# Performance work log

Hardware: AMD Instinct MI355X
Metric: run time of the kernel (lower is better)

## Reference

```python
import jax, jax.numpy as jnp
import numpy as np

N = 50000
E = 800000
IN_FEATS = 128
OUT_FEATS = 16
EDGE_FEATS = 1
NUM_HEADS = 8


def setup_inputs() -> dict:
    key = jax.random.key(0)
    ks = jax.random.split(key, 8)

    def xavier(k, shape):
        fan_in, fan_out = shape[-1], shape[-2] if len(shape) > 1 else shape[-1]
        bound = float(np.sqrt(6.0 / (shape[0] + shape[1])))
        return jax.random.uniform(k, shape, jnp.float32, -bound, bound)

    h = jax.random.normal(ks[0], (N, IN_FEATS), jnp.float32)
    edge_index = jax.random.randint(ks[1], (2, E), 0, N, jnp.int32)
    edge_feat = jax.random.normal(ks[2], (E, EDGE_FEATS), jnp.float32)
    # W_node stored as [in_feats, out_feats*num_heads] so h @ W_node == torch Linear(h)
    W_node = xavier(ks[3], (IN_FEATS, OUT_FEATS * NUM_HEADS))
    W_edge = xavier(ks[4], (EDGE_FEATS, NUM_HEADS))
    a_src = xavier(ks[5], (NUM_HEADS, OUT_FEATS))
    a_dst = xavier(ks[6], (NUM_HEADS, OUT_FEATS))
    return {"h": h, "edge_index": edge_index, "edge_feat": edge_feat,
            "W_node": W_node, "W_edge": W_edge, "a_src": a_src, "a_dst": a_dst}


def reference(h, edge_index, edge_feat, W_node, W_edge, a_src, a_dst):
    n = h.shape[0]
    src, dst = edge_index[0], edge_index[1]
    # node projection: [N, H, F]
    h_trans = (h @ W_node).reshape(n, NUM_HEADS, OUT_FEATS)
    # edge projection: [E, H]
    e_trans = edge_feat @ W_edge
    src_feat = h_trans[src]  # [E, H, F]
    dst_feat = h_trans[dst]  # [E, H, F]
    attn = (src_feat * a_src).sum(-1) + (dst_feat * a_dst).sum(-1) + e_trans  # [E, H]
    attn = jax.nn.leaky_relu(attn, negative_slope=0.2)
    # segment softmax over edges grouped by dst
    max_val = jax.ops.segment_max(attn, dst, num_segments=n)  # [N, H]
    exp_attn = jnp.exp(attn - max_val[dst])
    sum_exp = jax.ops.segment_sum(exp_attn, dst, num_segments=n)  # [N, H]
    alpha = exp_attn / jnp.maximum(sum_exp[dst], 1e-12)  # [E, H]
    msg = src_feat * alpha[..., None]  # [E, H, F]
    out = jax.ops.segment_sum(msg, dst, num_segments=n)  # [N, H, F]
    return out.mean(axis=1)  # [N, F]
```

## Files before the change

### kernel.cpp

```cpp
#include <hip/hip_runtime.h>

#define N_NODES 50000
#define N_EDGES 800000
#define IN_F    128
#define HEADS   8
#define OUT_F   16
#define NB_PROJ 782
#define NB_HIST 3125

typedef unsigned short u16;
typedef __attribute__((ext_vector_type(8))) short bf16x8;
typedef __attribute__((ext_vector_type(4))) float f32x4;

__device__ __forceinline__ float bf2f(u16 u) {
    return __uint_as_float(((unsigned)u) << 16);
}
__device__ __forceinline__ u16 f2bf(float f) {
    unsigned u = __float_as_uint(f);
    unsigned r = 0x7fffu + ((u >> 16) & 1u);
    return (u16)((u + r) >> 16);
}
__device__ __forceinline__ float ldf(const void* p, int i, bool bf) {
    return bf ? bf2f(((const u16*)p)[i]) : ((const float*)p)[i];
}

__global__ void probe_dtype(const void* __restrict__ h, int* __restrict__ flag) {
    if (threadIdx.x == 0 && blockIdx.x == 0) {
        const u16* u = (const u16*)h;
        int cnt = 0;
        for (int i = 0; i < 128; ++i) {
            int e = (u[i] >> 7) & 0xFF;
            if (e >= 90 && e <= 141) cnt++;
        }
        *flag = (cnt >= 110) ? 1 : 0;
    }
}

#define WT_STRIDE 136
__global__ __launch_bounds__(256) void proj_hist(
    const void* __restrict__ h, const void* __restrict__ Wn,
    const void* __restrict__ a_srcp, const void* __restrict__ a_dstp,
    const int* __restrict__ flag, const int* __restrict__ ei,
    u16* __restrict__ ht, float* __restrict__ s_src, float* __restrict__ s_dst,
    int* __restrict__ deg, int* __restrict__ rank)
{
    if (blockIdx.x >= NB_PROJ) {
        int e = (blockIdx.x - NB_PROJ) * 256 + threadIdx.x;
        if (e < N_EDGES) rank[e] = atomicAdd(&deg[ei[N_EDGES + e]], 1);
        return;
    }

    const bool bf = (*flag) != 0;
    __shared__ u16 Wsh[IN_F * WT_STRIDE];
    __shared__ float a_sh[2][IN_F];
    const int tid = threadIdx.x;

    if (tid < 128) a_sh[0][tid] = ldf(a_srcp, tid, bf);
    else           a_sh[1][tid - 128] = ldf(a_dstp, tid - 128, bf);

    {
        const int c8  = (tid & 15) * 8;
        const int kof = tid >> 4;
        const int ksw = (tid & 7) << 3;
        bf16x8 wv[8];
        if (bf) {
            const u16* wp = (const u16*)Wn;
            #pragma unroll
            for (int j = 0; j < 8; ++j)
                wv[j] = *(const bf16x8*)(wp + (size_t)(j * 16 + kof) * IN_F + c8);
        } else {
            const float* wp = (const float*)Wn;
            #pragma unroll
            for (int j = 0; j < 8; ++j) {
                const float* rp = wp + (size_t)(j * 16 + kof) * IN_F + c8;
                float4 fa = *(const float4*)(rp);
                float4 fb = *(const float4*)(rp + 4);
                bf16x8 t;
                t[0] = (short)f2bf(fa.x); t[1] = (short)f2bf(fa.y);
                t[2] = (short)f2bf(fa.z); t[3] = (short)f2bf(fa.w);
                t[4] = (short)f2bf(fb.x); t[5] = (short)f2bf(fb.y);
                t[6] = (short)f2bf(fb.z); t[7] = (short)f2bf(fb.w);
                wv[j] = t;
            }
        }
        #pragma unroll
        for (int j = 0; j < 8; ++j) {
            int kk = (j * 16 + kof) ^ ksw;
            #pragma unroll
            for (int jj = 0; jj < 8; ++jj)
                Wsh[(c8 + jj) * WT_STRIDE + kk] = (u16)wv[j][jj];
        }
    }
    __syncthreads();

    const int wave = tid >> 6, lane = tid & 63;
    const int m = lane & 15, q = lane >> 4;
    const int row_t = blockIdx.x * 64 + wave * 16;

    bf16x8 afr[4];
    int arow = row_t + m;
    if (arow >= N_NODES) arow = N_NODES - 1;
    if (bf) {
        const u16* hp = (const u16*)h + (size_t)arow * IN_F;
        #pragma unroll
        for (int kt = 0; kt < 4; ++kt)
            afr[kt] = *(const bf16x8*)(hp + kt * 32 + q * 8);
    } else {
        const float* hp = (const float*)h + (size_t)arow * IN_F;
        #pragma unroll
        for (int kt = 0; kt < 4; ++kt) {
            bf16x8 t;
            #pragma unroll
            for (int j = 0; j < 8; ++j) t[j] = (short)f2bf(hp[kt * 32 + q * 8 + j]);
            afr[kt] = t;
        }
    }

    f32x4 accs[8];
    #pragma unroll
    for (int ct = 0; ct < 8; ++ct) {
        const int csw = ((2 * ct + (m >> 3)) & 7) << 3;
        f32x4 acc = {0.f, 0.f, 0.f, 0.f};
        #pragma unroll
        for (int kt = 0; kt < 4; ++kt) {
            bf16x8 bfr = *(const bf16x8*)(Wsh + (ct * 16 + m) * WT_STRIDE
                                          + ((kt * 32 + q * 8) ^ csw));
            acc = __builtin_amdgcn_mfma_f32_16x16x32_bf16(afr[kt], bfr, acc, 0, 0, 0);
        }
        accs[ct] = acc;
    }

    __syncthreads();

    const int wbase = wave * 16;
    #pragma unroll
    for (int ct = 0; ct < 8; ++ct)
        #pragma unroll
        for (int r = 0; r < 4; ++r)
            Wsh[(wbase + q * 4 + r) * WT_STRIDE + ct * 16 + m] = f2bf(accs[ct][r]);

    const int r2 = lane & 15, hp2 = lane >> 4;
    const int grow = row_t + r2;
    const u16* wrow = Wsh + (wbase + r2) * WT_STRIDE;
    bf16x8 h0 = *(const bf16x8*)(wrow + hp2 * 32);
    bf16x8 h1 = *(const bf16x8*)(wrow + hp2 * 32 + 8);
    bf16x8 h2 = *(const bf16x8*)(wrow + hp2 * 32 + 16);
    bf16x8 h3 = *(const bf16x8*)(wrow + hp2 * 32 + 24);

    if (grow < N_NODES) {
        u16* hb = ht + (size_t)grow * IN_F + hp2 * 32;
        *(bf16x8*)(hb)      = h0;
        *(bf16x8*)(hb + 8)  = h1;
        *(bf16x8*)(hb + 16) = h2;
        *(bf16x8*)(hb + 24) = h3;
    }

    #pragma unroll
    for (int hh = 0; hh < 2; ++hh) {
        const int hd = hp2 * 2 + hh;
        float s1 = 0.f, s2 = 0.f;
        #pragma unroll
        for (int f = 0; f < 8; ++f) {
            float xa = bf2f((u16)((hh == 0) ? h0[f] : h2[f]));
            float xb = bf2f((u16)((hh == 0) ? h1[f] : h3[f]));
            s1 = fmaf(xa, a_sh[0][hd * 16 + f], s1);
            s1 = fmaf(xb, a_sh[0][hd * 16 + 8 + f], s1);
            s2 = fmaf(xa, a_sh[1][hd * 16 + f], s2);
            s2 = fmaf(xb, a_sh[1][hd * 16 + 8 + f], s2);
        }
        if (grow < N_NODES) {
            s_src[grow * HEADS + hd] = s1;
            s_dst[grow * HEADS + hd] = s2;
        }
    }
}

__global__ __launch_bounds__(1024) void scan_deg(const int* __restrict__ deg,
                                                 int* __restrict__ csr) {
    __shared__ int wsums[16];
    const int tid = threadIdx.x, lane = tid & 63, wid = tid >> 6;
    const int base = tid * 52;

    int s = 0;
    for (int c = 0; c < 13; ++c) {
        int idx = base + c * 4;
        if (idx + 3 < N_NODES) {
            int4 q = *(const int4*)(deg + idx);
            s += q.x + q.y + q.z + q.w;
        } else {
            for (int j = 0; j < 4; ++j)
                if (idx + j < N_NODES) s += deg[idx + j];
        }
    }

    int x = s;
    #pragma unroll
    for (int o = 1; o < 64; o <<= 1) {
        int y = __shfl_up(x, o, 64);
        if (lane >= o) x += y;
    }
    if (lane == 63) wsums[wid] = x;
    __syncthreads();
    if (wid == 0) {
        int v = (lane < 16) ? wsums[lane] : 0;
        #pragma unroll
        for (int o = 1; o < 16; o <<= 1) {
            int y = __shfl_up(v, o, 16);
            if ((lane & 15) >= o) v += y;
        }
        if (lane < 16) wsums[lane] = v;
    }
    __syncthreads();
    int run = ((wid > 0) ? wsums[wid - 1] : 0) + (x - s);

    for (int c = 0; c < 13; ++c) {
        int idx = base + c * 4;
        if (idx + 3 < N_NODES) {
            int4 q = *(const int4*)(deg + idx);
            int4 o4 = {run, run + q.x, run + q.x + q.y, run + q.x + q.y + q.z};
            *(int4*)(csr + idx) = o4;
            run += q.x + q.y + q.z + q.w;
        } else {
            for (int j = 0; j < 4; ++j)
                if (idx + j < N_NODES) { csr[idx + j] = run; run += deg[idx + j]; }
        }
    }
    if (tid == 1023) csr[N_NODES] = run;
}

__global__ __launch_bounds__(256) void scatter_edges(
    const int* __restrict__ ei, const void* __restrict__ ef,
    const int* __restrict__ flag, const int* __restrict__ rank,
    const int* __restrict__ csr, int2* __restrict__ edges)
{
    const bool bf = (*flag) != 0;
    int e = blockIdx.x * 256 + threadIdx.x;
    if (e >= N_EDGES) return;
    int src = ei[e];
    int dst = ei[N_EDGES + e];
    int pos = csr[dst] + rank[e];
    float efv = ldf(ef, e, bf);
    edges[pos] = make_int2(src, __float_as_int(efv));
}

__global__ __launch_bounds__(256) void fused_aggregate(
    const int* __restrict__ csr, const int2* __restrict__ edges,
    const void* __restrict__ We,
    const float* __restrict__ s_src, const float* __restrict__ s_dst,
    const u16* __restrict__ ht, const int* __restrict__ flag,
    void* __restrict__ out)
{
    const bool bf = (*flag) != 0;
    int g = blockIdx.x * 32 + (threadIdx.x >> 3);
    if (g >= N_NODES) return;
    const int hd = threadIdx.x & 7;
    int beg = csr[g], end = csr[g + 1];
    const float dval = s_dst[g * HEADS + hd];
    const float wev = ldf(We, hd, bf);

    float num[16];
    #pragma unroll
    for (int f = 0; f < 16; ++f) num[f] = 0.f;
    float den = 0.f;

    int2 eN = make_int2(0, 0);
    float svN = 0.f;
    bf16x8 v0N = {0,0,0,0,0,0,0,0}, v1N = {0,0,0,0,0,0,0,0};
    if (beg < end) {
        eN = edges[beg];
        svN = s_src[eN.x * HEADS + hd];
        const u16* hp = ht + (size_t)eN.x * IN_F + hd * 16;
        v0N = *(const bf16x8*)hp;
        v1N = *(const bf16x8*)(hp + 8);
    }
    for (int i = beg; i < end; ++i) {
        int2 eC = eN;
        float sv = svN;
        bf16x8 v0 = v0N, v1 = v1N;
        if (i + 1 < end) {
            eN = edges[i + 1];
            svN = s_src[eN.x * HEADS + hd];
            const u16* hp = ht + (size_t)eN.x * IN_F + hd * 16;
            v0N = *(const bf16x8*)hp;
            v1N = *(const bf16x8*)(hp + 8);
        }
        float a = sv + dval + __int_as_float(eC.y) * wev;
        a = (a > 0.f) ? a : 0.2f * a;
        float ex = __expf(a);
        den += ex;
        #pragma unroll
        for (int f = 0; f < 8; ++f) {
            num[f]     = fmaf(ex, bf2f((u16)v0[f]), num[f]);
            num[8 + f] = fmaf(ex, bf2f((u16)v1[f]), num[8 + f]);
        }
    }

    float rc = 1.0f / fmaxf(den, 1e-12f);
    #pragma unroll
    for (int f = 0; f < 16; ++f) num[f] *= rc;
    #pragma unroll
    for (int o = 1; o < 8; o <<= 1)
        #pragma unroll
        for (int f = 0; f < 16; ++f)
            num[f] += __shfl_xor(num[f], o, 8);

    float o0 = num[2 * hd] * 0.125f;
    float o1 = num[2 * hd + 1] * 0.125f;
    if (bf) {
        unsigned pw = ((unsigned)f2bf(o1) << 16) | (unsigned)f2bf(o0);
        *(unsigned*)((u16*)out + (size_t)g * OUT_F + hd * 2) = pw;
    } else {
        float2 f2v = {o0, o1};
        *(float2*)((float*)out + (size_t)g * OUT_F + hd * 2) = f2v;
    }
}

extern "C" void kernel_launch(void* const* d_in, const int* in_sizes, int n_in,
                              void* d_out, int out_size, void* d_ws, size_t ws_size,
                              hipStream_t stream) {
    const void* h     = d_in[0];
    const int*  ei    = (const int*)d_in[1];
    const void* efeat = d_in[2];
    const void* Wn    = d_in[3];
    const void* We    = d_in[4];
    const void* a_src = d_in[5];
    const void* a_dst = d_in[6];

    char* ws = (char*)d_ws;
    int*   flag    = (int*)ws;   ws += 256;
    u16*   ht      = (u16*)ws;   ws += (size_t)N_NODES * IN_F * 2;
    float* s_src   = (float*)ws; ws += (size_t)N_NODES * HEADS * 4;
    float* s_dst   = (float*)ws; ws += (size_t)N_NODES * HEADS * 4;
    int*   deg     = (int*)ws;   ws += (size_t)50048 * 4;
    int*   csr     = (int*)ws;   ws += (size_t)50048 * 4;
    int*   rank    = (int*)ws;   ws += (size_t)N_EDGES * 4;
    int2*  edges   = (int2*)ws;  ws += (size_t)N_EDGES * 8;

    hipLaunchKernelGGL(probe_dtype, dim3(1), dim3(64), 0, stream, h, flag);
    hipMemsetAsync(deg, 0, (size_t)N_NODES * 4, stream);
    hipLaunchKernelGGL(proj_hist, dim3(NB_PROJ + NB_HIST), dim3(256),
                       0, stream, h, Wn, a_src, a_dst, flag, ei,
                       ht, s_src, s_dst, deg, rank);
    hipLaunchKernelGGL(scan_deg, dim3(1), dim3(1024), 0, stream, deg, csr);
    hipLaunchKernelGGL(scatter_edges, dim3((N_EDGES + 255) / 256), dim3(256),
                       0, stream, ei, efeat, flag, rank, csr, edges);
    hipLaunchKernelGGL(fused_aggregate, dim3((N_NODES + 31) / 32), dim3(256),
                       0, stream, csr, edges, We, s_src, s_dst, ht, flag, d_out);
}
```

Baseline: 213.1 us.

## Fuse dtype probe and deg zeroing, pre-transpose weights, unroll aggregation by four

Replaces the single-thread dtype probe kernel and the memset with one init kernel that zeroes the degree array and writes a transposed bf16 copy of W_node. Each later kernel re-derives the dtype flag with a wave ballot instead of reading it from the workspace. The projection blocks now read B fragments straight from the global transposed weight, so the per-block 34KB LDS transpose and its barrier go away and LDS holds only a small per-wave staging tile. The aggregation loop drops its one-ahead prefetch in favour of a 4-way unrolled gather to put more loads in flight. The cost is a redundant probe in every block and weight loads that now go through global memory and cache.

```diff
diff --git a/kernel.cpp b/kernel.cpp
--- a/kernel.cpp
+++ b/kernel.cpp
@@ -7,6 +7,8 @@
 #define OUT_F   16
 #define NB_PROJ 782
 #define NB_HIST 3125
+#define NB_ZERO 196
+#define NB_WT   64
 
 typedef unsigned short u16;
 typedef __attribute__((ext_vector_type(8))) short bf16x8;
@@ -24,23 +26,42 @@
     return bf ? bf2f(((const u16*)p)[i]) : ((const float*)p)[i];
 }
 
-__global__ void probe_dtype(const void* __restrict__ h, int* __restrict__ flag) {
-    if (threadIdx.x == 0 && blockIdx.x == 0) {
+__device__ __forceinline__ bool probe_bf(const void* h, int tid, int* bf_sh) {
+    if (tid < 64) {
         const u16* u = (const u16*)h;
-        int cnt = 0;
-        for (int i = 0; i < 128; ++i) {
-            int e = (u[i] >> 7) & 0xFF;
-            if (e >= 90 && e <= 141) cnt++;
-        }
-        *flag = (cnt >= 110) ? 1 : 0;
-    }
-}
-
-#define WT_STRIDE 136
+        int e1 = (u[tid] >> 7) & 0xFF;
+        int e2 = (u[tid + 64] >> 7) & 0xFF;
+        unsigned long long b1 = __ballot(e1 >= 90 && e1 <= 141);
+        unsigned long long b2 = __ballot(e2 >= 90 && e2 <= 141);
+        if (tid == 0) *bf_sh = (__popcll(b1) + __popcll(b2) >= 110) ? 1 : 0;
+    }
+    __syncthreads();
+    return *bf_sh != 0;
+}
+
+__global__ __launch_bounds__(256) void init_ws(const void* __restrict__ h,
+                                               const void* __restrict__ Wn,
+                                               int* __restrict__ deg,
+                                               u16* __restrict__ WT) {
+    const int tid = threadIdx.x, bid = blockIdx.x;
+    if (bid < NB_ZERO) {
+        int i = bid * 256 + tid;
+        if (i < N_NODES) deg[i] = 0;
+        return;
+    }
+    __shared__ int bf_sh;
+    const bool bf = probe_bf(h, tid, &bf_sh);
+    int i = (bid - NB_ZERO) * 256 + tid;
+    int k = i >> 7, c = i & 127;
+    u16 v = bf ? ((const u16*)Wn)[i] : f2bf(((const float*)Wn)[i]);
+    WT[c * IN_F + k] = v;
+}
+
+#define TS_STRIDE 144
 __global__ __launch_bounds__(256) void proj_hist(
-    const void* __restrict__ h, const void* __restrict__ Wn,
+    const void* __restrict__ h, const u16* __restrict__ WT,
     const void* __restrict__ a_srcp, const void* __restrict__ a_dstp,
-    const int* __restrict__ flag, const int* __restrict__ ei,
+    const int* __restrict__ ei,
     u16* __restrict__ ht, float* __restrict__ s_src, float* __restrict__ s_dst,
     int* __restrict__ deg, int* __restrict__ rank)
 {
@@ -50,48 +71,14 @@
         return;
     }
 
-    const bool bf = (*flag) != 0;
-    __shared__ u16 Wsh[IN_F * WT_STRIDE];
+    __shared__ u16 Tsh[4][16 * TS_STRIDE];
     __shared__ float a_sh[2][IN_F];
+    __shared__ int bf_sh;
     const int tid = threadIdx.x;
+    const bool bf = probe_bf(h, tid, &bf_sh);
 
     if (tid < 128) a_sh[0][tid] = ldf(a_srcp, tid, bf);
     else           a_sh[1][tid - 128] = ldf(a_dstp, tid - 128, bf);
-
-    {
-        const int c8  = (tid & 15) * 8;
-        const int kof = tid >> 4;
-        const int ksw = (tid & 7) << 3;
-        bf16x8 wv[8];
-        if (bf) {
-            const u16* wp = (const u16*)Wn;
-            #pragma unroll
-            for (int j = 0; j < 8; ++j)
-                wv[j] = *(const bf16x8*)(wp + (size_t)(j * 16 + kof) * IN_F + c8);
-        } else {
-            const float* wp = (const float*)Wn;
-            #pragma unroll
-            for (int j = 0; j < 8; ++j) {
-                const float* rp = wp + (size_t)(j * 16 + kof) * IN_F + c8;
-                float4 fa = *(const float4*)(rp);
-                float4 fb = *(const float4*)(rp + 4);
-                bf16x8 t;
-                t[0] = (short)f2bf(fa.x); t[1] = (short)f2bf(fa.y);
-                t[2] = (short)f2bf(fa.z); t[3] = (short)f2bf(fa.w);
-                t[4] = (short)f2bf(fb.x); t[5] = (short)f2bf(fb.y);
-                t[6] = (short)f2bf(fb.z); t[7] = (short)f2bf(fb.w);
-                wv[j] = t;
-            }
-        }
-        #pragma unroll
-        for (int j = 0; j < 8; ++j) {
-            int kk = (j * 16 + kof) ^ ksw;
-            #pragma unroll
-            for (int jj = 0; jj < 8; ++jj)
-                Wsh[(c8 + jj) * WT_STRIDE + kk] = (u16)wv[j][jj];
-        }
-    }
-    __syncthreads();
 
     const int wave = tid >> 6, lane = tid & 63;
     const int m = lane & 15, q = lane >> 4;
@@ -119,29 +106,28 @@
     f32x4 accs[8];
     #pragma unroll
     for (int ct = 0; ct < 8; ++ct) {
-        const int csw = ((2 * ct + (m >> 3)) & 7) << 3;
+        const u16* wr = WT + (size_t)(ct * 16 + m) * IN_F;
         f32x4 acc = {0.f, 0.f, 0.f, 0.f};
         #pragma unroll
         for (int kt = 0; kt < 4; ++kt) {
-            bf16x8 bfr = *(const bf16x8*)(Wsh + (ct * 16 + m) * WT_STRIDE
-                                          + ((kt * 32 + q * 8) ^ csw));
+            bf16x8 bfr = *(const bf16x8*)(wr + kt * 32 + q * 8);
             acc = __builtin_amdgcn_mfma_f32_16x16x32_bf16(afr[kt], bfr, acc, 0, 0, 0);
         }
         accs[ct] = acc;
     }
 
+    u16* ts = Tsh[wave];
+    #pragma unroll
+    for (int ct = 0; ct < 8; ++ct)
+        #pragma unroll
+        for (int r = 0; r < 4; ++r)
+            ts[(q * 4 + r) * TS_STRIDE + ct * 16 + m] = f2bf(accs[ct][r]);
+
     __syncthreads();
-
-    const int wbase = wave * 16;
-    #pragma unroll
-    for (int ct = 0; ct < 8; ++ct)
-        #pragma unroll
-        for (int r = 0; r < 4; ++r)
-            Wsh[(wbase + q * 4 + r) * WT_STRIDE + ct * 16 + m] = f2bf(accs[ct][r]);
 
     const int r2 = lane & 15, hp2 = lane >> 4;
     const int grow = row_t + r2;
-    const u16* wrow = Wsh + (wbase + r2) * WT_STRIDE;
+    const u16* wrow = ts + r2 * TS_STRIDE;
     bf16x8 h0 = *(const bf16x8*)(wrow + hp2 * 32);
     bf16x8 h1 = *(const bf16x8*)(wrow + hp2 * 32 + 8);
     bf16x8 h2 = *(const bf16x8*)(wrow + hp2 * 32 + 16);
@@ -154,7 +140,6 @@
         *(bf16x8*)(hb + 16) = h2;
         *(bf16x8*)(hb + 24) = h3;
     }
-
     #pragma unroll
     for (int hh = 0; hh < 2; ++hh) {
         const int hd = hp2 * 2 + hh;
@@ -229,11 +214,12 @@
 }
 
 __global__ __launch_bounds__(256) void scatter_edges(
-    const int* __restrict__ ei, const void* __restrict__ ef,
-    const int* __restrict__ flag, const int* __restrict__ rank,
+    const void* __restrict__ h, const int* __restrict__ ei,
+    const void* __restrict__ ef, const int* __restrict__ rank,
     const int* __restrict__ csr, int2* __restrict__ edges)
 {
-    const bool bf = (*flag) != 0;
+    __shared__ int bf_sh;
+    const bool bf = probe_bf(h, threadIdx.x, &bf_sh);
     int e = blockIdx.x * 256 + threadIdx.x;
     if (e >= N_EDGES) return;
     int src = ei[e];
@@ -244,13 +230,14 @@
 }
 
 __global__ __launch_bounds__(256) void fused_aggregate(
+    const void* __restrict__ h,
     const int* __restrict__ csr, const int2* __restrict__ edges,
     const void* __restrict__ We,
     const float* __restrict__ s_src, const float* __restrict__ s_dst,
-    const u16* __restrict__ ht, const int* __restrict__ flag,
-    void* __restrict__ out)
+    const u16* __restrict__ ht, void* __restrict__ out)
 {
-    const bool bf = (*flag) != 0;
+    __shared__ int bf_sh;
+    const bool bf = probe_bf(h, threadIdx.x, &bf_sh);
     int g = blockIdx.x * 32 + (threadIdx.x >> 3);
     if (g >= N_NODES) return;
     const int hd = threadIdx.x & 7;
@@ -263,27 +250,48 @@
     for (int f = 0; f < 16; ++f) num[f] = 0.f;
     float den = 0.f;
 
-    int2 eN = make_int2(0, 0);
-    float svN = 0.f;
-    bf16x8 v0N = {0,0,0,0,0,0,0,0}, v1N = {0,0,0,0,0,0,0,0};
-    if (beg < end) {
-        eN = edges[beg];
-        svN = s_src[eN.x * HEADS + hd];
-        const u16* hp = ht + (size_t)eN.x * IN_F + hd * 16;
-        v0N = *(const bf16x8*)hp;
-        v1N = *(const bf16x8*)(hp + 8);
-    }
-    for (int i = beg; i < end; ++i) {
-        int2 eC = eN;
-        float sv = svN;
-        bf16x8 v0 = v0N, v1 = v1N;
-        if (i + 1 < end) {
-            eN = edges[i + 1];
-            svN = s_src[eN.x * HEADS + hd];
-            const u16* hp = ht + (size_t)eN.x * IN_F + hd * 16;
-            v0N = *(const bf16x8*)hp;
-            v1N = *(const bf16x8*)(hp + 8);
-        }
+    int i = beg;
+    for (; i + 4 <= end; i += 4) {
+        int2 ea = edges[i], eb = edges[i + 1], ec = edges[i + 2], ed = edges[i + 3];
+        float sa = s_src[ea.x * HEADS + hd];
+        float sb = s_src[eb.x * HEADS + hd];
+        float sc = s_src[ec.x * HEADS + hd];
+        float sd = s_src[ed.x * HEADS + hd];
+        const u16* pa = ht + (size_t)ea.x * IN_F + hd * 16;
+        const u16* pb = ht + (size_t)eb.x * IN_F + hd * 16;
+        const u16* pc = ht + (size_t)ec.x * IN_F + hd * 16;
+        const u16* pd = ht + (size_t)ed.x * IN_F + hd * 16;
+        bf16x8 va0 = *(const bf16x8*)pa, va1 = *(const bf16x8*)(pa + 8);
+        bf16x8 vb0 = *(const bf16x8*)pb, vb1 = *(const bf16x8*)(pb + 8);
+        bf16x8 vc0 = *(const bf16x8*)pc, vc1 = *(const bf16x8*)(pc + 8);
+        bf16x8 vd0 = *(const bf16x8*)pd, vd1 = *(const bf16x8*)(pd + 8);
+        float aa = sa + dval + __int_as_float(ea.y) * wev;
+        float ab = sb + dval + __int_as_float(eb.y) * wev;
+        float ac = sc + dval + __int_as_float(ec.y) * wev;
+        float ad = sd + dval + __int_as_float(ed.y) * wev;
+        aa = (aa > 0.f) ? aa : 0.2f * aa;
+        ab = (ab > 0.f) ? ab : 0.2f * ab;
+        ac = (ac > 0.f) ? ac : 0.2f * ac;
+        ad = (ad > 0.f) ? ad : 0.2f * ad;
+        float xa = __expf(aa), xb = __expf(ab), xc = __expf(ac), xd = __expf(ad);
+        den += (xa + xb) + (xc + xd);
+        #pragma unroll
+        for (int f = 0; f < 8; ++f) {
+            num[f]     = fmaf(xa, bf2f((u16)va0[f]), num[f]);
+            num[8 + f] = fmaf(xa, bf2f((u16)va1[f]), num[8 + f]);
+            num[f]     = fmaf(xb, bf2f((u16)vb0[f]), num[f]);
+            num[8 + f] = fmaf(xb, bf2f((u16)vb1[f]), num[8 + f]);
+            num[f]     = fmaf(xc, bf2f((u16)vc0[f]), num[f]);
+            num[8 + f] = fmaf(xc, bf2f((u16)vc1[f]), num[8 + f]);
+            num[f]     = fmaf(xd, bf2f((u16)vd0[f]), num[f]);
+            num[8 + f] = fmaf(xd, bf2f((u16)vd1[f]), num[8 + f]);
+        }
+    }
+    for (; i < end; ++i) {
+        int2 eC = edges[i];
+        float sv = s_src[eC.x * HEADS + hd];
+        const u16* hp = ht + (size_t)eC.x * IN_F + hd * 16;
+        bf16x8 v0 = *(const bf16x8*)hp, v1 = *(const bf16x8*)(hp + 8);
         float a = sv + dval + __int_as_float(eC.y) * wev;
         a = (a > 0.f) ? a : 0.2f * a;
         float ex = __expf(a);
@@ -327,23 +335,23 @@
     const void* a_dst = d_in[6];
 
     char* ws = (char*)d_ws;
-    int*   flag    = (int*)ws;   ws += 256;
     u16*   ht      = (u16*)ws;   ws += (size_t)N_NODES * IN_F * 2;
-    float* s_src   = (float*)ws; ws += (size_t)N_NODES * HEADS * 4;
-    float* s_dst   = (float*)ws; ws += (size_t)N_NODES * HEADS * 4;
+    float* s_srcp  = (float*)ws; ws += (size_t)N_NODES * HEADS * 4;
+    float* s_dstp  = (float*)ws; ws += (size_t)N_NODES * HEADS * 4;
     int*   deg     = (int*)ws;   ws += (size_t)50048 * 4;
     int*   csr     = (int*)ws;   ws += (size_t)50048 * 4;
     int*   rank    = (int*)ws;   ws += (size_t)N_EDGES * 4;
+    u16*   WT      = (u16*)ws;   ws += (size_t)IN_F * IN_F * 2;
     int2*  edges   = (int2*)ws;  ws += (size_t)N_EDGES * 8;
 
-    hipLaunchKernelGGL(probe_dtype, dim3(1), dim3(64), 0, stream, h, flag);
-    hipMemsetAsync(deg, 0, (size_t)N_NODES * 4, stream);
+    hipLaunchKernelGGL(init_ws, dim3(NB_ZERO + NB_WT), dim3(256),
+                       0, stream, h, Wn, deg, WT);
     hipLaunchKernelGGL(proj_hist, dim3(NB_PROJ + NB_HIST), dim3(256),
-                       0, stream, h, Wn, a_src, a_dst, flag, ei,
-                       ht, s_src, s_dst, deg, rank);
+                       0, stream, h, WT, a_src, a_dst, ei,
+                       ht, s_srcp, s_dstp, deg, rank);
     hipLaunchKernelGGL(scan_deg, dim3(1), dim3(1024), 0, stream, deg, csr);
     hipLaunchKernelGGL(scatter_edges, dim3((N_EDGES + 255) / 256), dim3(256),
-                       0, stream, ei, efeat, flag, rank, csr, edges);
+                       0, stream, h, ei, efeat, rank, csr, edges);
     hipLaunchKernelGGL(fused_aggregate, dim3((N_NODES + 31) / 32), dim3(256),
-                       0, stream, csr, edges, We, s_src, s_dst, ht, flag, d_out);
-}
+                       0, stream, h, csr, edges, We, s_srcp, s_dstp, ht, d_out);
+}
```

After: 214.2 us. No clear change (+0.5%).
